# Optimization experiments

Measured on AMD Instinct MI355X. Metric: run time of the kernel, lower is better.

The kernel has to match this reference:

```python
import jax, jax.numpy as jnp
import numpy as np

NUM_SELECT = 128  # num_select['layer1']


def setup_inputs() -> dict:
    key = jax.random.key(0)
    k1, k2 = jax.random.split(key)
    B, S, C, NC = 32, 4096, 256, 200
    x = jax.random.normal(k1, (B, S, C), dtype=jnp.float32)
    W = jax.random.normal(k2, (C, NC), dtype=jnp.float32) * (1.0 / np.sqrt(C))
    b = jnp.zeros((NC,), dtype=jnp.float32)
    return {"x": x, "W": W, "b": b}


def reference(x, W, b):
    # x: [B, S, C]; classifier logits: [B, S, NC]
    logits = jnp.einsum('bsc,cn->bsn', x, W) + b
    probs = jax.nn.softmax(logits, axis=-1)
    # per-token max class probability -> [B, S]
    max_ids = jnp.max(probs, axis=-1)
    # sort tokens per sample by confidence, descending (vectorized over batch)
    ranks = jnp.argsort(-max_ids, axis=-1)          # [B, S]
    top = ranks[:, :NUM_SELECT]                     # [B, num_select]
    # gather selected token features -> [B, num_select, C]
    selections = jnp.take_along_axis(x, top[:, :, None], axis=1)
    return selections
```

## Files before the change

### kernel.cpp

```cpp
#include <hip/hip_runtime.h>
#include <stdint.h>

#define CDIM 256
#define NCLS 200
#define NSEL 128
#define SEQ  4096
#define RPB  16
#define CCH  32

__device__ __forceinline__ float np_expf(float x) {
    const float LOG2E = 1.442695040888963407359924681001892137f;
    const float MAGIC = 12582912.0f;
    const float CW_HI = -6.93145752e-1f;
    const float CW_LO = -1.42860677e-6f;

    float q = __fsub_rn(__fmaf_rn(x, LOG2E, MAGIC), MAGIC);

    float y = __fmaf_rn(q, CW_HI, x);
    y = __fmaf_rn(q, CW_LO, y);

    float num = __fmaf_rn(5.082762527590693718096e-04f, y,
                          6.757896990527504603057e-03f);
    num = __fmaf_rn(num, y, 5.114512081637298353406e-02f);
    num = __fmaf_rn(num, y, 2.473615434895520810817e-01f);
    num = __fmaf_rn(num, y, 7.257664613233124478488e-01f);
    num = __fmaf_rn(num, y, 9.999999999980870924916e-01f);

    float den = __fmaf_rn(2.159509375685829852307e-02f, y,
                          -2.742335390411667452936e-01f);
    den = __fmaf_rn(den, y, 1.0f);

    const float r = __fdiv_rn(num, den);
    return ldexpf(r, (int)q);
}

__global__ __launch_bounds__(256) void score_kernel(
    const float* __restrict__ x, const float* __restrict__ W,
    const float* __restrict__ bias, float* __restrict__ scores)
{
    __shared__ __align__(16) float xs[RPB * CDIM];
    __shared__ __align__(16) float wtb[CCH * NCLS];
    __shared__ float mx[RPB][16];
    __shared__ float sp[RPB][16];
    __shared__ float mrow[RPB];

    const int tid = threadIdx.x;
    const long long row0 = (long long)blockIdx.x * RPB;

    {
        const float4* xg = reinterpret_cast<const float4*>(x + row0 * CDIM);
        float4* xs4 = reinterpret_cast<float4*>(xs);
        for (int i = tid; i < RPB * CDIM / 4; i += 256) xs4[i] = xg[i];
    }

    const int rg = tid / 50;
    const int q  = tid - rg * 50;
    const bool active = (tid < 200);

    float acc[4][4][8];
    #pragma unroll
    for (int r = 0; r < 4; ++r)
        #pragma unroll
        for (int k = 0; k < 4; ++k)
            #pragma unroll
            for (int j = 0; j < 8; ++j) acc[r][k][j] = 0.0f;

    for (int cc = 0; cc < CDIM; cc += CCH) {
        __syncthreads();
        {
            const float4* wg = reinterpret_cast<const float4*>(W + cc * NCLS);
            float4* wt4 = reinterpret_cast<float4*>(wtb);
            for (int i = tid; i < CCH * NCLS / 4; i += 256) wt4[i] = wg[i];
        }
        __syncthreads();

        if (active) {
            #pragma unroll
            for (int i = 3; i >= 0; --i) {
                float4 xq0[4], xq1[4];
                #pragma unroll
                for (int r = 0; r < 4; ++r) {
                    const float* xrow = &xs[(rg * 4 + r) * CDIM + cc + 8 * i];
                    xq0[r] = *reinterpret_cast<const float4*>(xrow);
                    xq1[r] = *reinterpret_cast<const float4*>(xrow + 4);
                }
                #pragma unroll
                for (int j = 0; j < 8; ++j) {
                    const float4 wv = *reinterpret_cast<const float4*>(
                        &wtb[(8 * i + j) * NCLS + 4 * q]);
                    #pragma unroll
                    for (int r = 0; r < 4; ++r) {
                        const float xv = (j < 4)
                            ? reinterpret_cast<const float*>(&xq0[r])[j]
                            : reinterpret_cast<const float*>(&xq1[r])[j - 4];
                        acc[r][0][j] = __fmaf_rn(xv, wv.x, acc[r][0][j]);
                        acc[r][1][j] = __fmaf_rn(xv, wv.y, acc[r][1][j]);
                        acc[r][2][j] = __fmaf_rn(xv, wv.z, acc[r][2][j]);
                        acc[r][3][j] = __fmaf_rn(xv, wv.w, acc[r][3][j]);
                    }
                }
            }
        }
    }
    __syncthreads();
    float* lg = wtb;

    if (active) {
        const float4 bq = reinterpret_cast<const float4*>(bias)[q];
        const float bv[4] = { bq.x, bq.y, bq.z, bq.w };
        #pragma unroll
        for (int r = 0; r < 4; ++r) {
            float h[4];
            #pragma unroll
            for (int k = 0; k < 4; ++k) {
                const float* a = acc[r][k];
                h[k] = __fadd_rn(
                    __fadd_rn(__fadd_rn(a[0], a[1]), __fadd_rn(a[2], a[3])),
                    __fadd_rn(__fadd_rn(a[4], a[5]), __fadd_rn(a[6], a[7])));
                h[k] = __fadd_rn(h[k], bv[k]);
            }
            *reinterpret_cast<float4*>(&lg[(rg * 4 + r) * NCLS + 4 * q]) =
                make_float4(h[0], h[1], h[2], h[3]);
        }
    }
    __syncthreads();

    {
        const int r = tid >> 4, l = tid & 15;
        float mv = lg[r * NCLS + l];
        for (int n = l + 16; n < NCLS; n += 16) mv = fmaxf(mv, lg[r * NCLS + n]);
        mx[r][l] = mv;
    }
    __syncthreads();
    if (tid < RPB) {
        float mv = mx[tid][0];
        #pragma unroll
        for (int l = 1; l < 16; ++l) mv = fmaxf(mv, mx[tid][l]);
        mrow[tid] = mv;
    }
    __syncthreads();

    for (int i = tid; i < RPB * NCLS; i += 256) {
        const int r = i / NCLS;
        lg[i] = np_expf(__fsub_rn(lg[i], mrow[r]));
    }
    __syncthreads();

    {
        const int r = tid >> 4, sub = tid & 15;
        const int k = sub & 7, blk = sub >> 3;
        const float* a = &lg[r * NCLS + (blk ? 96 : 0)];
        const int len = blk ? 104 : 96;
        float c = a[k];
        for (int i = 8; i < len; i += 8) c = __fadd_rn(c, a[i + k]);
        sp[r][blk * 8 + k] = c;
    }
    __syncthreads();

    if (tid < RPB) {
        const float* p = sp[tid];
        const float s1 =
            __fadd_rn(__fadd_rn(__fadd_rn(p[0], p[1]), __fadd_rn(p[2], p[3])),
                      __fadd_rn(__fadd_rn(p[4], p[5]), __fadd_rn(p[6], p[7])));
        const float s2 =
            __fadd_rn(__fadd_rn(__fadd_rn(p[8], p[9]), __fadd_rn(p[10], p[11])),
                      __fadd_rn(__fadd_rn(p[12], p[13]), __fadd_rn(p[14], p[15])));
        const float S = __fadd_rn(s1, s2);
        scores[row0 + tid] = __fdiv_rn(1.0f, S);
    }
}

__global__ __launch_bounds__(256) void sort_gather_kernel(
    const float* __restrict__ pmax, const float* __restrict__ x,
    float* __restrict__ out)
{
    __shared__ uint64_t K[SEQ];

    const int tid = threadIdx.x;
    const int b   = blockIdx.x;

    for (int i = tid; i < SEQ; i += 256) {
        const uint32_t pb = __float_as_uint(pmax[(long long)b * SEQ + i]);
        K[i] = ((uint64_t)pb << 12) | (uint64_t)(SEQ - 1 - i);
    }
    __syncthreads();

    for (int k = 2; k <= SEQ; k <<= 1) {
        for (int j = k >> 1; j > 0; j >>= 1) {
            for (int t = tid; t < SEQ / 2; t += 256) {
                const int i = ((t & ~(j - 1)) << 1) | (t & (j - 1));
                const int p = i | j;
                const bool desc = ((i & k) == 0);
                const uint64_t a = K[i], c = K[p];
                const bool sw = desc ? (a < c) : (a > c);
                if (sw) { K[i] = c; K[p] = a; }
            }
            __syncthreads();
        }
    }

    const float4* x4   = reinterpret_cast<const float4*>(x);
    float4*       out4 = reinterpret_cast<float4*>(out);
    for (int t = tid; t < NSEL * (CDIM / 4); t += 256) {
        const int jj = t >> 6;
        const int c4 = t & 63;
        const int idx = (SEQ - 1) - (int)(K[jj] & (uint64_t)(SEQ - 1));
        out4[((long long)b * NSEL + jj) * (CDIM / 4) + c4] =
            x4[((long long)b * SEQ + idx) * (CDIM / 4) + c4];
    }
}

extern "C" void kernel_launch(void* const* d_in, const int* in_sizes, int n_in,
                              void* d_out, int out_size, void* d_ws, size_t ws_size,
                              hipStream_t stream) {
    const float* x    = (const float*)d_in[0];
    const float* W    = (const float*)d_in[1];
    const float* bias = (const float*)d_in[2];
    float* out   = (float*)d_out;
    float* score = (float*)d_ws;

    const long long nrows = (long long)in_sizes[0] / CDIM;
    const int B = out_size / (NSEL * CDIM);

    score_kernel<<<(int)(nrows / RPB), 256, 0, stream>>>(x, W, bias, score);
    sort_gather_kernel<<<B, 256, 0, stream>>>(score, x, out);
}
```

Measured before the change: 437.7 us.

## Double-buffer W chunks via direct global-to-LDS loads in score kernel

Replaces the register-staged copies of x and W into shared memory with global_load_lds async transfers that write straight into LDS. W chunks are double-buffered so the next chunk's load is issued before computing on the current one, which removes one barrier per chunk and overlaps the load with the FMAs. This doubles W's LDS footprint, which may lower occupancy, and it relies on the barrier waiting for the outstanding LDS-targeted loads.

```diff
diff --git a/kernel.cpp b/kernel.cpp
--- a/kernel.cpp
+++ b/kernel.cpp
@@ -34,24 +34,38 @@
     return ldexpf(r, (int)q);
 }
 
+static __device__ __forceinline__ void gl_lds16(const float* g, float* lds_base) {
+    __builtin_amdgcn_global_load_lds(
+        (const __attribute__((address_space(1))) void*)g,
+        (__attribute__((address_space(3))) void*)lds_base, 16, 0, 0);
+}
+
 __global__ __launch_bounds__(256) void score_kernel(
     const float* __restrict__ x, const float* __restrict__ W,
     const float* __restrict__ bias, float* __restrict__ scores)
 {
     __shared__ __align__(16) float xs[RPB * CDIM];
-    __shared__ __align__(16) float wtb[CCH * NCLS];
+    __shared__ __align__(16) float wtb[2][CCH * NCLS];
     __shared__ float mx[RPB][16];
     __shared__ float sp[RPB][16];
     __shared__ float mrow[RPB];
 
-    const int tid = threadIdx.x;
+    const int tid  = threadIdx.x;
+    const int wid  = tid >> 6;
+    const int lane = tid & 63;
     const long long row0 = (long long)blockIdx.x * RPB;
 
     {
-        const float4* xg = reinterpret_cast<const float4*>(x + row0 * CDIM);
-        float4* xs4 = reinterpret_cast<float4*>(xs);
-        for (int i = tid; i < RPB * CDIM / 4; i += 256) xs4[i] = xg[i];
-    }
+        const float* xg = x + row0 * CDIM;
+        for (int t = wid; t < RPB * CDIM / 256; t += 4)
+            gl_lds16(xg + (t * 64 + lane) * 4, &xs[t * 256]);
+    }
+    {
+        const float* wg = W;
+        for (int t = wid; t < CCH * NCLS / 256; t += 4)
+            gl_lds16(wg + (t * 64 + lane) * 4, &wtb[0][t * 256]);
+    }
+    __syncthreads();
 
     const int rg = tid / 50;
     const int q  = tid - rg * 50;
@@ -65,16 +79,17 @@
             #pragma unroll
             for (int j = 0; j < 8; ++j) acc[r][k][j] = 0.0f;
 
-    for (int cc = 0; cc < CDIM; cc += CCH) {
-        __syncthreads();
-        {
-            const float4* wg = reinterpret_cast<const float4*>(W + cc * NCLS);
-            float4* wt4 = reinterpret_cast<float4*>(wtb);
-            for (int i = tid; i < CCH * NCLS / 4; i += 256) wt4[i] = wg[i];
-        }
-        __syncthreads();
+    for (int c8 = 0; c8 < CDIM / CCH; ++c8) {
+        const int cur = c8 & 1;
+        if (c8 < CDIM / CCH - 1) {
+            const float* wg = W + (long long)(c8 + 1) * CCH * NCLS;
+            for (int t = wid; t < CCH * NCLS / 256; t += 4)
+                gl_lds16(wg + (t * 64 + lane) * 4, &wtb[cur ^ 1][t * 256]);
+        }
 
         if (active) {
+            const float* wt = wtb[cur];
+            const int cc = c8 * CCH;
             #pragma unroll
             for (int i = 3; i >= 0; --i) {
                 float4 xq0[4], xq1[4];
@@ -87,7 +102,7 @@
                 #pragma unroll
                 for (int j = 0; j < 8; ++j) {
                     const float4 wv = *reinterpret_cast<const float4*>(
-                        &wtb[(8 * i + j) * NCLS + 4 * q]);
+                        &wt[(8 * i + j) * NCLS + 4 * q]);
                     #pragma unroll
                     for (int r = 0; r < 4; ++r) {
                         const float xv = (j < 4)
@@ -101,9 +116,10 @@
                 }
             }
         }
-    }
-    __syncthreads();
-    float* lg = wtb;
+        __syncthreads();
+    }
+
+    float* lg = wtb[0];
 
     if (active) {
         const float4 bq = reinterpret_cast<const float4*>(bias)[q];
```

New measurement: 565.2 us. 1.29x slower.
